# Kernel tuning notes

Measured on AMD Instinct MI355X. Metric: run time of the kernel, lower is better.

The kernel has to match this reference:

```python
import jax, jax.numpy as jnp
import numpy as np

EMBED_DIM = 1152
NUM_HEADS = 16
HEAD_DIM = EMBED_DIM // NUM_HEADS  # 72
SCALE = HEAD_DIM ** -0.5


def setup_inputs() -> dict:
    key = jax.random.key(0)
    ks = jax.random.split(key, 5)
    B, S, D = 32, 729, EMBED_DIM
    hidden_states = jax.random.normal(ks[0], (B, S, D), dtype=jnp.float32)
    # fused QKV projection weight/bias (q|k|v concatenated on output dim)
    w_qkv = jax.random.normal(ks[1], (D, 3 * D), dtype=jnp.float32) * (D ** -0.5)
    b_qkv = jax.random.normal(ks[2], (3 * D,), dtype=jnp.float32) * 0.02
    w_out = jax.random.normal(ks[3], (D, D), dtype=jnp.float32) * (D ** -0.5)
    b_out = jax.random.normal(ks[4], (D,), dtype=jnp.float32) * 0.02
    return {"hidden_states": hidden_states, "w_qkv": w_qkv, "b_qkv": b_qkv,
            "w_out": w_out, "b_out": b_out}


def reference(hidden_states, w_qkv, b_qkv, w_out, b_out):
    B, S, D = hidden_states.shape
    qkv = hidden_states @ w_qkv + b_qkv              # [B,S,3D]
    q, k, v = jnp.split(qkv, 3, axis=-1)
    # [B,S,D] -> [B,H,S,hd]
    def to_heads(x):
        return x.reshape(B, S, NUM_HEADS, HEAD_DIM).transpose(0, 2, 1, 3)
    q, k, v = to_heads(q), to_heads(k), to_heads(v)
    scores = jnp.einsum('bhqd,bhkd->bhqk', q, k) * SCALE
    attn = jax.nn.softmax(scores, axis=-1)
    out = jnp.einsum('bhqk,bhkd->bhqd', attn, v)     # [B,H,S,hd]
    out = out.transpose(0, 2, 1, 3).reshape(B, S, D)
    return out @ w_out + b_out
```

## Files before the change

### kernel.cpp

```cpp
#include <hip/hip_runtime.h>
#include <hip/hip_bf16.h>
#include <stdint.h>

typedef unsigned short u16;
typedef __attribute__((ext_vector_type(8))) short bf16x8;
typedef __attribute__((ext_vector_type(4))) float f32x4;
typedef __attribute__((ext_vector_type(4))) unsigned short us4;

#define T_TOK   23328
#define MPAD    23424
#define DMODEL  1152
#define N3      3456
#define NHEAD   16
#define HDIM    72
#define SEQ     729
#define VSTR    736
#define SCALE_F 0.1178511301977579f

__device__ __forceinline__ u16 f2bf(float f) {
  unsigned u = __builtin_bit_cast(unsigned, f);
  u += 0x7fffu + ((u >> 16) & 1u);
  return (u16)(u >> 16);
}

__device__ __forceinline__ f32x4 mfma16(bf16x8 a, bf16x8 b, f32x4 c) {
  return __builtin_amdgcn_mfma_f32_16x16x32_bf16(a, b, c, 0, 0, 0);
}

#define GL16(g, l)                                                        \
  __builtin_amdgcn_global_load_lds(                                       \
      (const __attribute__((address_space(1))) void*)(g),                 \
      (__attribute__((address_space(3))) void*)(l), 16, 0, 0)


__global__ void k_cvt_hidden(const float* __restrict__ in, u16* __restrict__ out) {
  size_t i4 = ((size_t)blockIdx.x * blockDim.x + threadIdx.x) * 4;
  if (i4 >= (size_t)MPAD * DMODEL) return;
  us4 o;
  if (i4 < (size_t)T_TOK * DMODEL) {
    float4 v = *(const float4*)(in + i4);
    o[0] = f2bf(v.x); o[1] = f2bf(v.y); o[2] = f2bf(v.z); o[3] = f2bf(v.w);
  } else {
    o[0] = 0; o[1] = 0; o[2] = 0; o[3] = 0;
  }
  *(us4*)(out + i4) = o;
}

template <int R, int C>
__global__ void k_transpose(const float* __restrict__ w, u16* __restrict__ wt) {
  size_t i = (size_t)blockIdx.x * blockDim.x + threadIdx.x;
  if (i >= (size_t)R * C) return;
  int n  = (int)(i / R);
  int kk = (int)(i - (size_t)n * R);
  wt[i] = f2bf(w[(size_t)kk * C + n]);
}

template <int EPI>
__global__ __launch_bounds__(256) void k_gemm(
    const u16* __restrict__ A, const u16* __restrict__ Bt,
    const float* __restrict__ bias,
    u16* __restrict__ qo, u16* __restrict__ ko, u16* __restrict__ vTo,
    float* __restrict__ outp)
{
  __shared__ u16 As[128 * 32];
  __shared__ u16 Bs[128 * 32];
  const int tid  = threadIdx.x;
  const int wave = tid >> 6;
  const int lane = tid & 63;
  const int m0 = blockIdx.y * 128;
  const int n0 = blockIdx.x * 128;
  const int wm = (wave >> 1) * 64;
  const int wn = (wave & 1) * 64;

  const int rofs = wave * 16 + (lane >> 2);
  const int cofs = (lane & 3) * 8;
  const u16* gA0 = A  + (size_t)(m0 + rofs) * DMODEL + cofs;
  const u16* gA1 = gA0 + (size_t)64 * DMODEL;
  const u16* gB0 = Bt + (size_t)(n0 + rofs) * DMODEL + cofs;
  const u16* gB1 = gB0 + (size_t)64 * DMODEL;
  char* lA0 = (char*)As + wave * 1024;
  char* lA1 = (char*)As + 4096 + wave * 1024;
  char* lB0 = (char*)Bs + wave * 1024;
  char* lB1 = (char*)Bs + 4096 + wave * 1024;

  const int fr = lane & 15;
  const int fk = (lane >> 4) * 8;

  f32x4 acc[4][4] = {};

  for (int kt = 0; kt < DMODEL; kt += 32) {
    GL16(gA0 + kt, lA0);
    GL16(gA1 + kt, lA1);
    GL16(gB0 + kt, lB0);
    GL16(gB1 + kt, lB1);
    __syncthreads();
    bf16x8 af[4], bfrag[4];
#pragma unroll
    for (int i = 0; i < 4; ++i)
      af[i] = *(const bf16x8*)&As[(wm + i * 16 + fr) * 32 + fk];
#pragma unroll
    for (int j = 0; j < 4; ++j)
      bfrag[j] = *(const bf16x8*)&Bs[(wn + j * 16 + fr) * 32 + fk];
#pragma unroll
    for (int i = 0; i < 4; ++i)
#pragma unroll
      for (int j = 0; j < 4; ++j)
        acc[i][j] = mfma16(af[i], bfrag[j], acc[i][j]);
    __syncthreads();
  }

#pragma unroll
  for (int j = 0; j < 4; ++j) {
    const int n = n0 + wn + j * 16 + fr;
    const float bi = bias[n];
    if (EPI == 0) {
      const int which = n / DMODEL;
      const int rr = n - which * DMODEL;
      const int h = rr / HDIM;
      const int d = rr - h * HDIM;
#pragma unroll
      for (int i = 0; i < 4; ++i) {
        const int tr = m0 + wm + i * 16 + (lane >> 4) * 4;
#pragma unroll
        for (int rg = 0; rg < 4; ++rg) {
          const int t = tr + rg;
          if (t < T_TOK) {
            const int bb = t / SEQ;
            const int s  = t - bb * SEQ;
            const int bh = bb * NHEAD + h;
            const float val = acc[i][j][rg] + bi;
            if (which == 0)
              qo[((size_t)bh * SEQ + s) * HDIM + d] = f2bf(val * SCALE_F);
            else if (which == 1)
              ko[((size_t)bh * SEQ + s) * HDIM + d] = f2bf(val);
            else
              vTo[((size_t)bh * HDIM + d) * VSTR + s] = f2bf(val);
          }
        }
      }
    } else {
#pragma unroll
      for (int i = 0; i < 4; ++i) {
        const int tr = m0 + wm + i * 16 + (lane >> 4) * 4;
#pragma unroll
        for (int rg = 0; rg < 4; ++rg) {
          const int t = tr + rg;
          if (t < T_TOK)
            outp[(size_t)t * DMODEL + n] = acc[i][j][rg] + bi;
        }
      }
    }
  }
}

__global__ __launch_bounds__(64) void k_attn(
    const u16* __restrict__ q, const u16* __restrict__ k,
    const u16* __restrict__ vT, u16* __restrict__ aout)
{
  const int lane = threadIdx.x;
  const int qt = blockIdx.x;
  const int bh = blockIdx.y;
  const int q0 = qt * 16;
  const int fr = lane & 15;
  const int fg = lane >> 4;
  const int fk = fg * 8;

  const u16* qb = q  + (size_t)bh * (SEQ * HDIM);
  const u16* kb = k  + (size_t)bh * (SEQ * HDIM);
  const u16* vb = vT + (size_t)bh * (HDIM * VSTR);

  __shared__ u16 pl[16][40];

  const int qrow = q0 + fr;
  const bool qv = qrow < SEQ;
  bf16x8 qf0 = {}, qf1 = {}, qf2 = {};
  if (qv) {
    const u16* qp = qb + (size_t)qrow * HDIM;
    qf0 = *(const bf16x8*)(qp + fk);
    qf1 = *(const bf16x8*)(qp + 32 + fk);
    if (fg == 0) qf2 = *(const bf16x8*)(qp + 64);
  }

  f32x4 oacc[5] = {};
  float mrun[4] = {-1e30f, -1e30f, -1e30f, -1e30f};
  float lrun[4] = {0.f, 0.f, 0.f, 0.f};

  for (int kt = 0; kt < SEQ; kt += 32) {
    f32x4 sc[2];
#pragma unroll
    for (int hh = 0; hh < 2; ++hh) {
      const int krow = kt + hh * 16 + fr;
      bf16x8 kf0 = {}, kf1 = {}, kf2 = {};
      if (krow < SEQ) {
        const u16* kp = kb + (size_t)krow * HDIM;
        kf0 = *(const bf16x8*)(kp + fk);
        kf1 = *(const bf16x8*)(kp + 32 + fk);
        if (fg == 0) kf2 = *(const bf16x8*)(kp + 64);
      }
      f32x4 z = {};
      z = mfma16(qf0, kf0, z);
      z = mfma16(qf1, kf1, z);
      z = mfma16(qf2, kf2, z);
      if (krow >= SEQ) { z[0] = -1e30f; z[1] = -1e30f; z[2] = -1e30f; z[3] = -1e30f; }
      sc[hh] = z;
    }
#pragma unroll
    for (int r = 0; r < 4; ++r) {
      float mx = fmaxf(sc[0][r], sc[1][r]);
      mx = fmaxf(mx, __shfl_xor(mx, 1));
      mx = fmaxf(mx, __shfl_xor(mx, 2));
      mx = fmaxf(mx, __shfl_xor(mx, 4));
      mx = fmaxf(mx, __shfl_xor(mx, 8));
      const float mnew = fmaxf(mrun[r], mx);
      const float resc = __expf(mrun[r] - mnew);
      mrun[r] = mnew;
      const float p0 = __expf(sc[0][r] - mnew);
      const float p1 = __expf(sc[1][r] - mnew);
      float ps = p0 + p1;
      ps += __shfl_xor(ps, 1);
      ps += __shfl_xor(ps, 2);
      ps += __shfl_xor(ps, 4);
      ps += __shfl_xor(ps, 8);
      lrun[r] = lrun[r] * resc + ps;
#pragma unroll
      for (int v = 0; v < 5; ++v) oacc[v][r] *= resc;
      pl[fg * 4 + r][fr]      = f2bf(p0);
      pl[fg * 4 + r][16 + fr] = f2bf(p1);
    }
    __syncthreads();
    const bf16x8 pa = *(const bf16x8*)&pl[fr][fk];
#pragma unroll
    for (int v = 0; v < 5; ++v) {
      const int d = v * 16 + fr;
      bf16x8 vf = {};
      if (d < HDIM)
        vf = *(const bf16x8*)(vb + (size_t)d * VSTR + kt + fk);
      oacc[v] = mfma16(pa, vf, oacc[v]);
    }
    __syncthreads();
  }

  const int bb = bh >> 4, h = bh & 15;
#pragma unroll
  for (int r = 0; r < 4; ++r) {
    const int row = q0 + fg * 4 + r;
    if (row < SEQ) {
      const float inv = 1.0f / lrun[r];
      u16* op = aout + (size_t)(bb * SEQ + row) * DMODEL + h * HDIM;
#pragma unroll
      for (int v = 0; v < 5; ++v) {
        const int d = v * 16 + fr;
        if (d < HDIM) op[d] = f2bf(oacc[v][r] * inv);
      }
    }
  }
}

extern "C" void kernel_launch(void* const* d_in, const int* in_sizes, int n_in,
                              void* d_out, int out_size, void* d_ws, size_t ws_size,
                              hipStream_t stream) {
  (void)in_sizes; (void)n_in; (void)out_size; (void)ws_size;
  const float* hs   = (const float*)d_in[0];
  const float* wqkv = (const float*)d_in[1];
  const float* bqkv = (const float*)d_in[2];
  const float* wout = (const float*)d_in[3];
  const float* bout = (const float*)d_in[4];
  float* out = (float*)d_out;

  u16* hbuf  = (u16*)d_ws;
  u16* wqkvT = hbuf  + (size_t)MPAD * DMODEL;
  u16* woutT = wqkvT + (size_t)N3 * DMODEL;
  u16* qb    = woutT + (size_t)DMODEL * DMODEL;
  u16* kb    = qb    + (size_t)512 * SEQ * HDIM;
  u16* vTb   = kb    + (size_t)512 * SEQ * HDIM;

  k_cvt_hidden<<<(MPAD * DMODEL / 4 + 255) / 256, 256, 0, stream>>>(hs, hbuf);
  k_transpose<DMODEL, N3><<<((size_t)DMODEL * N3 + 255) / 256, 256, 0, stream>>>(wqkv, wqkvT);
  k_transpose<DMODEL, DMODEL><<<((size_t)DMODEL * DMODEL + 255) / 256, 256, 0, stream>>>(wout, woutT);
  k_gemm<0><<<dim3(N3 / 128, MPAD / 128), 256, 0, stream>>>(hbuf, wqkvT, bqkv, qb, kb, vTb, nullptr);
  k_attn<<<dim3(46, 512), 64, 0, stream>>>(qb, kb, vTb, hbuf);
  k_gemm<1><<<dim3(DMODEL / 128, MPAD / 128), 256, 0, stream>>>(hbuf, woutT, bout,
                                                                nullptr, nullptr, nullptr, out);
}
```

Baseline: 1.039 ms.

## Share double-buffered K/V tiles in LDS across four waves in attention kernel

Result: faster. 882.9 us (-15.0%).

```diff
diff --git a/kernel.cpp b/kernel.cpp
--- a/kernel.cpp
+++ b/kernel.cpp
@@ -16,6 +16,9 @@
 #define SEQ     729
 #define VSTR    736
 #define SCALE_F 0.1178511301977579f
+#define KVB     64
+#define NT      12
+#define THR     8.0f
 
 __device__ __forceinline__ u16 f2bf(float f) {
   unsigned u = __builtin_bit_cast(unsigned, f);
@@ -153,28 +156,67 @@
   }
 }
 
-__global__ __launch_bounds__(64) void k_attn(
+
+__device__ __forceinline__ void stage_kv(const u16* __restrict__ kb, const u16* __restrict__ vb,
+                                         u16* KsB, u16* VsB, int kt, int wv, int lane) {
+#pragma unroll
+  for (int rdi = 0; rdi < 2; ++rdi) {
+    const int c0 = rdi * 256 + wv * 64;
+    {
+      const int c = c0 + lane;
+      const int row = c / 9;
+      const int off = (c - row * 9) * 8;
+      GL16(kb + (size_t)(kt + row) * HDIM + off, KsB + (size_t)c0 * 8);
+    }
+    {
+      const int c = c0 + lane;
+      const int d = c >> 3;
+      int off = kt + (((c & 7) ^ (d & 7)) << 3);
+      off = off > (VSTR - 8) ? (VSTR - 8) : off;
+      GL16(vb + (size_t)d * VSTR + off, VsB + (size_t)c0 * 8);
+    }
+  }
+  if (wv == 0) {
+    const int c = 512 + lane;
+    const int row = c / 9;
+    const int off = (c - row * 9) * 8;
+    GL16(kb + (size_t)(kt + row) * HDIM + off, KsB + (size_t)512 * 8);
+    const int d = c >> 3;
+    int voff = kt + (((c & 7) ^ (d & 7)) << 3);
+    voff = voff > (VSTR - 8) ? (VSTR - 8) : voff;
+    GL16(vb + (size_t)d * VSTR + voff, VsB + (size_t)512 * 8);
+  }
+}
+
+__global__ __launch_bounds__(256) void k_attn(
     const u16* __restrict__ q, const u16* __restrict__ k,
     const u16* __restrict__ vT, u16* __restrict__ aout)
 {
-  const int lane = threadIdx.x;
-  const int qt = blockIdx.x;
-  const int bh = blockIdx.y;
-  const int q0 = qt * 16;
+  __shared__ alignas(16) u16 Ks[2][4640];
+  __shared__ alignas(16) u16 Vs[2][5120];
+  __shared__ alignas(16) u16 pl[4][16][72];
+
+  const int tid  = threadIdx.x;
+  const int wv   = tid >> 6;
+  const int lane = tid & 63;
   const int fr = lane & 15;
   const int fg = lane >> 4;
   const int fk = fg * 8;
 
+  const int bh = blockIdx.y;
+  const int qbase = blockIdx.x * 64 + wv * 16;
+
   const u16* qb = q  + (size_t)bh * (SEQ * HDIM);
   const u16* kb = k  + (size_t)bh * (SEQ * HDIM);
   const u16* vb = vT + (size_t)bh * (HDIM * VSTR);
 
-  __shared__ u16 pl[16][40];
-
-  const int qrow = q0 + fr;
-  const bool qv = qrow < SEQ;
+  if (tid < 64) { Vs[0][4608 + tid] = 0x3F80; Vs[1][4608 + tid] = 0x3F80; }
+  for (int i = tid; i < 448; i += 256) { Vs[0][4672 + i] = 0; Vs[1][4672 + i] = 0; }
+  if (tid < 32) { Ks[0][4608 + tid] = 0; Ks[1][4608 + tid] = 0; }
+
+  const int qrow = qbase + fr;
   bf16x8 qf0 = {}, qf1 = {}, qf2 = {};
-  if (qv) {
+  if (qrow < SEQ) {
     const u16* qp = qb + (size_t)qrow * HDIM;
     qf0 = *(const bf16x8*)(qp + fk);
     qf1 = *(const bf16x8*)(qp + 32 + fk);
@@ -183,69 +225,92 @@
 
   f32x4 oacc[5] = {};
   float mrun[4] = {-1e30f, -1e30f, -1e30f, -1e30f};
-  float lrun[4] = {0.f, 0.f, 0.f, 0.f};
-
-  for (int kt = 0; kt < SEQ; kt += 32) {
-    f32x4 sc[2];
-#pragma unroll
-    for (int hh = 0; hh < 2; ++hh) {
-      const int krow = kt + hh * 16 + fr;
-      bf16x8 kf0 = {}, kf1 = {}, kf2 = {};
-      if (krow < SEQ) {
-        const u16* kp = kb + (size_t)krow * HDIM;
-        kf0 = *(const bf16x8*)(kp + fk);
-        kf1 = *(const bf16x8*)(kp + 32 + fk);
-        if (fg == 0) kf2 = *(const bf16x8*)(kp + 64);
-      }
+
+  stage_kv(kb, vb, Ks[0], Vs[0], 0, wv, lane);
+  __syncthreads();
+
+  int buf = 0;
+  for (int t = 0; t < NT; ++t) {
+    const int kt = t * KVB;
+    if (t + 1 < NT)
+      stage_kv(kb, vb, Ks[buf ^ 1], Vs[buf ^ 1], kt + KVB, wv, lane);
+
+    const char* kB = (const char*)Ks[buf];
+    f32x4 sc[4];
+#pragma unroll
+    for (int hh = 0; hh < 4; ++hh) {
+      const char* krow = kB + (hh * 16 + fr) * 144;
+      bf16x8 kf0 = *(const bf16x8*)(krow + fg * 16);
+      bf16x8 kf1 = *(const bf16x8*)(krow + 64 + fg * 16);
+      bf16x8 kf2 = *(const bf16x8*)(krow + 128 + fg * 16);
       f32x4 z = {};
       z = mfma16(qf0, kf0, z);
       z = mfma16(qf1, kf1, z);
       z = mfma16(qf2, kf2, z);
-      if (krow >= SEQ) { z[0] = -1e30f; z[1] = -1e30f; z[2] = -1e30f; z[3] = -1e30f; }
       sc[hh] = z;
     }
+    if (kt + KVB > SEQ) {
+#pragma unroll
+      for (int hh = 0; hh < 4; ++hh)
+        if (kt + hh * 16 + fr >= SEQ) {
+          sc[hh][0] = -1e30f; sc[hh][1] = -1e30f; sc[hh][2] = -1e30f; sc[hh][3] = -1e30f;
+        }
+    }
+
+    float tmx[4];
+    bool needs = false;
 #pragma unroll
     for (int r = 0; r < 4; ++r) {
-      float mx = fmaxf(sc[0][r], sc[1][r]);
-      mx = fmaxf(mx, __shfl_xor(mx, 1));
-      mx = fmaxf(mx, __shfl_xor(mx, 2));
-      mx = fmaxf(mx, __shfl_xor(mx, 4));
-      mx = fmaxf(mx, __shfl_xor(mx, 8));
-      const float mnew = fmaxf(mrun[r], mx);
-      const float resc = __expf(mrun[r] - mnew);
-      mrun[r] = mnew;
-      const float p0 = __expf(sc[0][r] - mnew);
-      const float p1 = __expf(sc[1][r] - mnew);
-      float ps = p0 + p1;
-      ps += __shfl_xor(ps, 1);
-      ps += __shfl_xor(ps, 2);
-      ps += __shfl_xor(ps, 4);
-      ps += __shfl_xor(ps, 8);
-      lrun[r] = lrun[r] * resc + ps;
-#pragma unroll
-      for (int v = 0; v < 5; ++v) oacc[v][r] *= resc;
-      pl[fg * 4 + r][fr]      = f2bf(p0);
-      pl[fg * 4 + r][16 + fr] = f2bf(p1);
-    }
+      tmx[r] = fmaxf(fmaxf(sc[0][r], sc[1][r]), fmaxf(sc[2][r], sc[3][r]));
+      needs |= (tmx[r] > mrun[r] + THR);
+    }
+    if (__any(needs)) {
+#pragma unroll
+      for (int r = 0; r < 4; ++r) {
+        float tm = tmx[r];
+        tm = fmaxf(tm, __shfl_xor(tm, 1));
+        tm = fmaxf(tm, __shfl_xor(tm, 2));
+        tm = fmaxf(tm, __shfl_xor(tm, 4));
+        tm = fmaxf(tm, __shfl_xor(tm, 8));
+        const float mnew = fmaxf(mrun[r], tm);
+        const float resc = __expf(mrun[r] - mnew);
+        mrun[r] = mnew;
+#pragma unroll
+        for (int v = 0; v < 5; ++v) oacc[v][r] *= resc;
+      }
+    }
+#pragma unroll
+    for (int r = 0; r < 4; ++r) {
+      const int prow = fg * 4 + r;
+#pragma unroll
+      for (int hh = 0; hh < 4; ++hh)
+        pl[wv][prow][hh * 16 + fr] = f2bf(__expf(sc[hh][r] - mrun[r]));
+    }
+
+    const bf16x8 pa0 = *(const bf16x8*)&pl[wv][fr][fk];
+    const bf16x8 pa1 = *(const bf16x8*)&pl[wv][fr][32 + fk];
+    const char* vB = (const char*)Vs[buf];
+    const int swz = (fr & 7) << 4;
+#pragma unroll
+    for (int v = 0; v < 5; ++v) {
+      const char* vrow = vB + (size_t)(v * 16 + fr) * 128;
+      bf16x8 vf0 = *(const bf16x8*)(vrow + ((fg * 16) ^ swz));
+      bf16x8 vf1 = *(const bf16x8*)(vrow + (((4 + fg) * 16) ^ swz));
+      oacc[v] = mfma16(pa0, vf0, oacc[v]);
+      oacc[v] = mfma16(pa1, vf1, oacc[v]);
+    }
+
     __syncthreads();
-    const bf16x8 pa = *(const bf16x8*)&pl[fr][fk];
-#pragma unroll
-    for (int v = 0; v < 5; ++v) {
-      const int d = v * 16 + fr;
-      bf16x8 vf = {};
-      if (d < HDIM)
-        vf = *(const bf16x8*)(vb + (size_t)d * VSTR + kt + fk);
-      oacc[v] = mfma16(pa, vf, oacc[v]);
-    }
-    __syncthreads();
+    buf ^= 1;
   }
 
   const int bb = bh >> 4, h = bh & 15;
 #pragma unroll
   for (int r = 0; r < 4; ++r) {
-    const int row = q0 + fg * 4 + r;
+    const int row = qbase + fg * 4 + r;
     if (row < SEQ) {
-      const float inv = 1.0f / lrun[r];
+      const float l = __shfl(oacc[4][r], (lane & 48) | 8);
+      const float inv = 1.0f / l;
       u16* op = aout + (size_t)(bb * SEQ + row) * DMODEL + h * HDIM;
 #pragma unroll
       for (int v = 0; v < 5; ++v) {
@@ -278,7 +343,7 @@
   k_transpose<DMODEL, N3><<<((size_t)DMODEL * N3 + 255) / 256, 256, 0, stream>>>(wqkv, wqkvT);
   k_transpose<DMODEL, DMODEL><<<((size_t)DMODEL * DMODEL + 255) / 256, 256, 0, stream>>>(wout, woutT);
   k_gemm<0><<<dim3(N3 / 128, MPAD / 128), 256, 0, stream>>>(hbuf, wqkvT, bqkv, qb, kb, vTb, nullptr);
-  k_attn<<<dim3(46, 512), 64, 0, stream>>>(qb, kb, vTb, hbuf);
+  k_attn<<<dim3(12, 512), 256, 0, stream>>>(qb, kb, vTb, hbuf);
   k_gemm<1><<<dim3(DMODEL / 128, MPAD / 128), 256, 0, stream>>>(hbuf, woutT, bout,
                                                                 nullptr, nullptr, nullptr, out);
 }
```
